# Optimization experiments

Hardware: AMD Instinct MI355X
Metric: run time of the kernel (lower is better)

## Reference

```python
import jax, jax.numpy as jnp
import numpy as np

L = 30  # SSA window size (module default)


def _ssa_groups1(xm):
    """pyts-style SSA with groups=1: full-SVD reconstruction of the
    trajectory (Hankel) matrix followed by anti-diagonal averaging.
    xm: [B, N] -> [B, N]
    """
    B, N = xm.shape
    K = N - L + 1
    # Hankel trajectory matrix: X[b, i, j] = xm[b, i + j], shape [B, L, K]
    idx = jnp.arange(L)[:, None] + jnp.arange(K)[None, :]
    X = xm[:, idx]
    # SVD and rank-L reconstruction (groups=1 sums ALL elementary matrices)
    U, s, Vt = jnp.linalg.svd(X, full_matrices=False)  # U:[B,L,L] s:[B,L] Vt:[B,L,K]
    Xr = jnp.einsum('blr,br,brk->blk', U, s, Vt)       # [B, L, K]
    # Anti-diagonal (Hankel) averaging: average Xr[i, j] over i + j = t
    seg = idx.reshape(-1)                               # [L*K] values in [0, N)
    sums = jax.vmap(lambda m: jax.ops.segment_sum(m.reshape(-1), seg, num_segments=N))(Xr)
    counts = jax.ops.segment_sum(jnp.ones(L * K, dtype=xm.dtype), seg, num_segments=N)
    return sums / counts                                # [B, N]


def setup_inputs() -> dict:
    key = jax.random.key(0)
    x = jax.random.normal(key, (256, 64, 2048), dtype=jnp.float32)
    return {"x": x}


def reference(x):
    # x: [B, C, N]
    xm = jnp.max(x, axis=1)                 # channel-max, [B, N]
    x_ss = _ssa_groups1(xm)                 # SSA round-trip, [B, N]
    # Original code detaches the SSA branch (CPU/numpy round trip)
    x_ss = jax.lax.stop_gradient(x_ss)
    gate = jax.nn.softmax(x_ss, axis=-1)[:, None, :]  # [B, 1, N]
    return gate * x                         # [B, C, N]
```

## Files before the change

### kernel.cpp

```cpp
#include <hip/hip_runtime.h>
#include <math.h>


#define B_DIM 256
#define C_DIM 64
#define N_DIM 2048
#define THREADS 512

__global__ __launch_bounds__(THREADS)
void ssa_gate_kernel(const float* __restrict__ x, float* __restrict__ out) {
    const int b = blockIdx.x;
    const int t = threadIdx.x;
    const int lane = t & 63;
    const int wid  = t >> 6;

    const size_t base = (size_t)b * (C_DIM * N_DIM);
    const float4* __restrict__ xb = (const float4*)(x + base);
    float4* __restrict__ ob = (float4*)(out + base);
    const int stride4 = N_DIM / 4;

    __shared__ float sred[8];

    float4 m;
    m.x = -INFINITY; m.y = -INFINITY; m.z = -INFINITY; m.w = -INFINITY;
    #pragma unroll 8
    for (int c = 0; c < C_DIM; ++c) {
        float4 v = xb[c * stride4 + t];
        m.x = fmaxf(m.x, v.x);
        m.y = fmaxf(m.y, v.y);
        m.z = fmaxf(m.z, v.z);
        m.w = fmaxf(m.w, v.w);
    }

    float tm = fmaxf(fmaxf(m.x, m.y), fmaxf(m.z, m.w));
    #pragma unroll
    for (int off = 32; off > 0; off >>= 1)
        tm = fmaxf(tm, __shfl_down(tm, off, 64));
    if (lane == 0) sred[wid] = tm;
    __syncthreads();
    float M = sred[0];
    #pragma unroll
    for (int i = 1; i < 8; ++i) M = fmaxf(M, sred[i]);
    __syncthreads();

    float4 e;
    e.x = __expf(m.x - M);
    e.y = __expf(m.y - M);
    e.z = __expf(m.z - M);
    e.w = __expf(m.w - M);
    float ts = (e.x + e.y) + (e.z + e.w);
    #pragma unroll
    for (int off = 32; off > 0; off >>= 1)
        ts += __shfl_down(ts, off, 64);
    if (lane == 0) sred[wid] = ts;
    __syncthreads();
    float S = 0.0f;
    #pragma unroll
    for (int i = 0; i < 8; ++i) S += sred[i];

    const float inv = 1.0f / S;
    float4 g;
    g.x = e.x * inv; g.y = e.y * inv; g.z = e.z * inv; g.w = e.w * inv;

    #pragma unroll 8
    for (int c = 0; c < C_DIM; ++c) {
        float4 v = xb[c * stride4 + t];
        float4 o;
        o.x = v.x * g.x;
        o.y = v.y * g.y;
        o.z = v.z * g.z;
        o.w = v.w * g.w;
        ob[c * stride4 + t] = o;
    }
}

extern "C" void kernel_launch(void* const* d_in, const int* in_sizes, int n_in,
                              void* d_out, int out_size, void* d_ws, size_t ws_size,
                              hipStream_t stream) {
    const float* x = (const float*)d_in[0];
    float* out = (float*)d_out;
    ssa_gate_kernel<<<B_DIM, THREADS, 0, stream>>>(x, out);
}
```

Baseline: 247.7 us.

## Split fused gate kernel into partial-max, softmax and multiply kernels

Replaces the single kernel, which ran one 512-thread block per batch row (only 256 blocks), with three kernels. The first computes channel-max partials over 16-row slabs across 1024 blocks. The second reduces those partials and computes the softmax gate per batch. The third multiplies x by the gate over 8192 blocks. The aim is to raise occupancy and memory-level parallelism on a bandwidth-bound workload, at the cost of two extra launches, a workspace round trip for partials and gate, and x being read in two separate passes that may not stay in cache.

Measured after the change: 252.5 us. Within noise of the previous version (+2.0%).

```diff
diff --git a/kernel.cpp b/kernel.cpp
--- a/kernel.cpp
+++ b/kernel.cpp
@@ -5,32 +5,51 @@
 #define B_DIM 256
 #define C_DIM 64
 #define N_DIM 2048
-#define THREADS 512
+#define COLS4 (N_DIM / 4)
+#define ROWS_PER_PB 16
+#define PB_PER_B (C_DIM / ROWS_PER_PB)
+#define NUM_PB (B_DIM * PB_PER_B)
 
-__global__ __launch_bounds__(THREADS)
-void ssa_gate_kernel(const float* __restrict__ x, float* __restrict__ out) {
-    const int b = blockIdx.x;
-    const int t = threadIdx.x;
+static __device__ __forceinline__ float4 max4(float4 a, float4 b) {
+    float4 r;
+    r.x = fmaxf(a.x, b.x); r.y = fmaxf(a.y, b.y);
+    r.z = fmaxf(a.z, b.z); r.w = fmaxf(a.w, b.w);
+    return r;
+}
+
+__global__ __launch_bounds__(256)
+void k1_partial_max(const float* __restrict__ x, float4* __restrict__ part) {
+    const int pb = blockIdx.x;
+    const int t  = threadIdx.x;
+    const float4* __restrict__ xb =
+        (const float4*)x + (size_t)pb * ROWS_PER_PB * COLS4;
+    float4 m0, m1;
+    m0.x = m0.y = m0.z = m0.w = -INFINITY;
+    m1 = m0;
+    #pragma unroll
+    for (int r = 0; r < ROWS_PER_PB; ++r) {
+        float4 a = xb[r * COLS4 + t];
+        float4 b = xb[r * COLS4 + t + 256];
+        m0 = max4(m0, a);
+        m1 = max4(m1, b);
+    }
+    part[(size_t)pb * COLS4 + t]       = m0;
+    part[(size_t)pb * COLS4 + t + 256] = m1;
+}
+
+__global__ __launch_bounds__(512)
+void k2_softmax(const float4* __restrict__ part, float4* __restrict__ gate) {
+    const int b    = blockIdx.x;
+    const int t    = threadIdx.x;
     const int lane = t & 63;
     const int wid  = t >> 6;
 
-    const size_t base = (size_t)b * (C_DIM * N_DIM);
-    const float4* __restrict__ xb = (const float4*)(x + base);
-    float4* __restrict__ ob = (float4*)(out + base);
-    const int stride4 = N_DIM / 4;
+    __shared__ float sred[16];
 
-    __shared__ float sred[8];
-
-    float4 m;
-    m.x = -INFINITY; m.y = -INFINITY; m.z = -INFINITY; m.w = -INFINITY;
-    #pragma unroll 8
-    for (int c = 0; c < C_DIM; ++c) {
-        float4 v = xb[c * stride4 + t];
-        m.x = fmaxf(m.x, v.x);
-        m.y = fmaxf(m.y, v.y);
-        m.z = fmaxf(m.z, v.z);
-        m.w = fmaxf(m.w, v.w);
-    }
+    const float4* __restrict__ pb = part + (size_t)b * PB_PER_B * COLS4;
+    float4 m = pb[t];
+    #pragma unroll
+    for (int p = 1; p < PB_PER_B; ++p) m = max4(m, pb[p * COLS4 + t]);
 
     float tm = fmaxf(fmaxf(m.x, m.y), fmaxf(m.z, m.w));
     #pragma unroll
@@ -41,7 +60,6 @@
     float M = sred[0];
     #pragma unroll
     for (int i = 1; i < 8; ++i) M = fmaxf(M, sred[i]);
-    __syncthreads();
 
     float4 e;
     e.x = __expf(m.x - M);
@@ -52,25 +70,31 @@
     #pragma unroll
     for (int off = 32; off > 0; off >>= 1)
         ts += __shfl_down(ts, off, 64);
-    if (lane == 0) sred[wid] = ts;
+    if (lane == 0) sred[8 + wid] = ts;
     __syncthreads();
     float S = 0.0f;
     #pragma unroll
-    for (int i = 0; i < 8; ++i) S += sred[i];
+    for (int i = 8; i < 16; ++i) S += sred[i];
 
     const float inv = 1.0f / S;
     float4 g;
     g.x = e.x * inv; g.y = e.y * inv; g.z = e.z * inv; g.w = e.w * inv;
+    gate[(size_t)b * COLS4 + t] = g;
+}
 
-    #pragma unroll 8
-    for (int c = 0; c < C_DIM; ++c) {
-        float4 v = xb[c * stride4 + t];
-        float4 o;
-        o.x = v.x * g.x;
-        o.y = v.y * g.y;
-        o.z = v.z * g.z;
-        o.w = v.w * g.w;
-        ob[c * stride4 + t] = o;
+__global__ __launch_bounds__(256)
+void k3_mul(const float4* __restrict__ x, const float4* __restrict__ gate,
+            float4* __restrict__ out) {
+    const size_t i0 = (size_t)blockIdx.x * 1024 + threadIdx.x;
+    #pragma unroll
+    for (int k = 0; k < 4; ++k) {
+        const size_t i4 = i0 + (size_t)k * 256;
+        float4 v = x[i4];
+        const int col = (int)(i4 & (COLS4 - 1));
+        const int b   = (int)(i4 >> 15);
+        float4 g = gate[(size_t)b * COLS4 + col];
+        v.x *= g.x; v.y *= g.y; v.z *= g.z; v.w *= g.w;
+        out[i4] = v;
     }
 }
 
@@ -79,5 +103,11 @@
                               hipStream_t stream) {
     const float* x = (const float*)d_in[0];
     float* out = (float*)d_out;
-    ssa_gate_kernel<<<B_DIM, THREADS, 0, stream>>>(x, out);
+
+    float4* part = (float4*)d_ws;
+    float4* gate = part + (size_t)NUM_PB * COLS4;
+
+    k1_partial_max<<<NUM_PB, 256, 0, stream>>>(x, part);
+    k2_softmax<<<B_DIM, 512, 0, stream>>>(part, gate);
+    k3_mul<<<8192, 256, 0, stream>>>((const float4*)x, gate, (float4*)out);
 }
```
